# Kernel optimization log

Measured on AMD Instinct MI355X. Metric: run time of the kernel, lower is better.

Reference implementation:

```python
import jax, jax.numpy as jnp
import numpy as np

B = 16384
LATENT = 16
HID = 512
STYLE = 64
D = 10  # num_domains


def setup_inputs() -> dict:
    key = jax.random.key(0)
    ks = jax.random.split(key, 20)
    s = 0.02
    inp = {
        "z": jax.random.normal(ks[0], (B, LATENT), jnp.float32),
        "y": jax.random.randint(ks[1], (B,), 0, D, jnp.int32),
        "W0": jax.random.normal(ks[2], (LATENT, HID), jnp.float32) * s,
        "b0": jnp.zeros((HID,), jnp.float32),
        "W1": jax.random.normal(ks[3], (HID, HID), jnp.float32) * s,
        "b1": jnp.zeros((HID,), jnp.float32),
        "W2": jax.random.normal(ks[4], (HID, HID), jnp.float32) * s,
        "b2": jnp.zeros((HID,), jnp.float32),
        "W3": jax.random.normal(ks[5], (HID, HID), jnp.float32) * s,
        "b3": jnp.zeros((HID,), jnp.float32),
        "Wu1": jax.random.normal(ks[6], (D, HID, HID), jnp.float32) * s,
        "bu1": jnp.zeros((D, HID), jnp.float32),
        "Wu2": jax.random.normal(ks[7], (D, HID, HID), jnp.float32) * s,
        "bu2": jnp.zeros((D, HID), jnp.float32),
        "Wu3": jax.random.normal(ks[8], (D, HID, HID), jnp.float32) * s,
        "bu3": jnp.zeros((D, HID), jnp.float32),
        "Wo": jax.random.normal(ks[9], (D, HID, STYLE), jnp.float32) * s,
        "bo": jnp.zeros((D, STYLE), jnp.float32),
    }
    return inp


def reference(z, y, W0, b0, W1, b1, W2, b2, W3, b3,
              Wu1, bu1, Wu2, bu2, Wu3, bu3, Wo, bo):
    # shared trunk
    h = jax.nn.relu(z @ W0 + b0)
    h = jax.nn.relu(h @ W1 + b1)
    h = jax.nn.relu(h @ W2 + b2)
    h = jax.nn.relu(h @ W3 + b3)            # [B, HID]
    # all unshared heads computed densely (as in the original torch.stack)
    t = jax.nn.relu(jnp.einsum('bh,dhk->bdk', h, Wu1) + bu1)   # [B, D, HID]
    t = jax.nn.relu(jnp.einsum('bdh,dhk->bdk', t, Wu2) + bu2)
    t = jax.nn.relu(jnp.einsum('bdh,dhk->bdk', t, Wu3) + bu3)
    out = jnp.einsum('bdh,dhk->bdk', t, Wo) + bo               # [B, D, STYLE]
    # gather the branch indexed by y for each sample
    s = out[jnp.arange(z.shape[0]), y]                          # [B, STYLE]
    return s
```

## Files before the change

kernel.cpp:

```cpp
#include <hip/hip_runtime.h>

#define NB 16384
#define NDOM 10
#define HIDN 512
#define STYLE 64
#define NWIN 256

typedef short bf16x8 __attribute__((ext_vector_type(8)));
typedef float f32x16 __attribute__((ext_vector_type(16)));

#define MFMA __builtin_amdgcn_mfma_f32_32x32x16_bf16


__device__ __forceinline__ unsigned bfr_hi(float x) {
    unsigned u = __float_as_uint(x);
    return (u + 0x7fffu + ((u >> 16) & 1u)) & 0xffff0000u;
}

__device__ __forceinline__ unsigned cvtpk(float a, float b) {
    unsigned r;
    asm("v_cvt_pk_bf16_f32 %0, %1, %2" : "=v"(r) : "v"(a), "v"(b));
    return r;
}

__device__ __forceinline__ void cvhalf2(const float4& x, const float4& y, uint4& h, uint4& l) {
    float xs[8] = {x.x, x.y, x.z, x.w, y.x, y.y, y.z, y.w};
    unsigned hh[8], ll[8];
#pragma unroll
    for (int i = 0; i < 8; ++i) {
        unsigned hb = bfr_hi(xs[i]);
        hh[i] = hb;
        ll[i] = bfr_hi(xs[i] - __uint_as_float(hb));
    }
    h = make_uint4((hh[0] >> 16) | (hh[1] & 0xffff0000u), (hh[2] >> 16) | (hh[3] & 0xffff0000u),
                   (hh[4] >> 16) | (hh[5] & 0xffff0000u), (hh[6] >> 16) | (hh[7] & 0xffff0000u));
    l = make_uint4((ll[0] >> 16) | (ll[1] & 0xffff0000u), (ll[2] >> 16) | (ll[3] & 0xffff0000u),
                   (ll[4] >> 16) | (ll[5] & 0xffff0000u), (ll[6] >> 16) | (ll[7] & 0xffff0000u));
}


__global__ void k_scatter(const int* __restrict__ y, const int* __restrict__ counts,
                          int* __restrict__ cursors, int* __restrict__ rowidx) {
    __shared__ int soff[NDOM];
    if (threadIdx.x == 0) {
        int s = 0;
        for (int dd = 0; dd < NDOM; ++dd) { soff[dd] = s; s += counts[dd]; }
    }
    __syncthreads();
    int b = blockIdx.x * 256 + threadIdx.x;
    int d = y[b];
    int lane = threadIdx.x & 63;
#pragma unroll
    for (int dd = 0; dd < NDOM; ++dd) {
        unsigned long long bal = __ballot(d == dd);
        if (bal == 0ULL) continue;
        int leader = __builtin_ctzll(bal);
        int base = 0;
        if (d == dd && lane == leader)
            base = atomicAdd(&cursors[dd], (int)__popcll(bal));
        base = __shfl(base, leader);
        if (d == dd) {
            int rank = (int)__popcll(bal & ((1ULL << lane) - 1ULL));
            rowidx[soff[dd] + base + rank] = b;
        }
    }
}


__global__ void k_prep(const float* __restrict__ W1, const float* __restrict__ W2,
                       const float* __restrict__ W3, const float* __restrict__ Wu1,
                       const float* __restrict__ Wu2, const float* __restrict__ Wu3,
                       const float* __restrict__ W0, const float* __restrict__ Wo,
                       const int* __restrict__ y,
                       short* __restrict__ Wp, short* __restrict__ W0p,
                       short* __restrict__ WoP, int* __restrict__ counts)
{
    const int b = blockIdx.x;
    const int t = threadIdx.x;
    if (b < 2112) {
        __shared__ float Ld[64][68];
        const int mat = b >> 6, wq = (b >> 3) & 7, s = b & 7;
        const float* src;
        if (mat < 3) src = (mat == 0 ? W1 : (mat == 1 ? W2 : W3));
        else {
            int g = (mat - 3) / 10, d = (mat - 3) % 10;
            src = (g == 0 ? Wu1 : (g == 1 ? Wu2 : Wu3)) + (size_t)d * HIDN * HIDN;
        }
        short* dst = Wp + (size_t)mat * 262144 + wq * 32768;
#pragma unroll
        for (int i = 0; i < 4; ++i) {
            int idx = i * 256 + t;
            int row = idx >> 4, c4 = idx & 15;
            *(float4*)&Ld[row][c4 * 4] =
                *(const float4*)(src + (size_t)(s * 64 + row) * HIDN + wq * 64 + c4 * 4);
        }
        __syncthreads();
#pragma unroll
        for (int i = 0; i < 2; ++i) {
            int g = i * 256 + t;
            int ksl = g >> 7, of = (g >> 6) & 1, k8 = (g >> 5) & 1, c5 = g & 31;
            int kk = ksl * 16 + k8 * 8;
            unsigned pk[4];
#pragma unroll
            for (int j2 = 0; j2 < 4; ++j2) {
                unsigned h0 = bfr_hi(Ld[kk + 2 * j2][of * 32 + c5]);
                unsigned h1 = bfr_hi(Ld[kk + 2 * j2 + 1][of * 32 + c5]);
                pk[j2] = (h0 >> 16) | (h1 & 0xffff0000u);
            }
            int ksg = s * 4 + ksl;
            *(uint4*)(dst + ksg * 1024 + of * 512 + k8 * 256 + c5 * 8) =
                make_uint4(pk[0], pk[1], pk[2], pk[3]);
        }
    } else if (b == 2112) {
#pragma unroll
        for (int i = 0; i < 4; ++i) {
            int g = i * 256 + t;
            int wq = g >> 7, of = (g >> 6) & 1, k8 = (g >> 5) & 1, c5 = g & 31;
            int col = wq * 64 + of * 32 + c5;
            unsigned pk[4];
#pragma unroll
            for (int j2 = 0; j2 < 4; ++j2) {
                unsigned h0 = bfr_hi(W0[(size_t)(k8 * 8 + 2 * j2) * HIDN + col]);
                unsigned h1 = bfr_hi(W0[(size_t)(k8 * 8 + 2 * j2 + 1) * HIDN + col]);
                pk[j2] = (h0 >> 16) | (h1 & 0xffff0000u);
            }
            *(uint4*)(W0p + g * 8) = make_uint4(pk[0], pk[1], pk[2], pk[3]);
        }
    } else if (b < 2123) {
        const int dom = b - 2113;
        const float* src = Wo + (size_t)dom * HIDN * STYLE;
        short* dst = WoP + (size_t)dom * 32768;
#pragma unroll
        for (int i = 0; i < 16; ++i) {
            int g = i * 256 + t;
            int w1 = g >> 11, ks = (g >> 6) & 31, k8 = (g >> 5) & 1, c5 = g & 31;
            int col = w1 * 32 + c5;
            int k0 = ks * 16 + k8 * 8;
            unsigned pk[4];
#pragma unroll
            for (int j2 = 0; j2 < 4; ++j2) {
                unsigned h0 = bfr_hi(src[(size_t)(k0 + 2 * j2) * STYLE + col]);
                unsigned h1 = bfr_hi(src[(size_t)(k0 + 2 * j2 + 1) * STYLE + col]);
                pk[j2] = (h0 >> 16) | (h1 & 0xffff0000u);
            }
            *(uint4*)(dst + g * 8) = make_uint4(pk[0], pk[1], pk[2], pk[3]);
        }
    } else {
        int idx = (b - 2123) * 256 + t;
        int d = y[idx];
        int lane = t & 63;
#pragma unroll
        for (int dd = 0; dd < NDOM; ++dd) {
            unsigned long long bal = __ballot(d == dd);
            if (bal != 0ULL && d == dd && lane == __builtin_ctzll(bal))
                atomicAdd(&counts[dd], (int)__popcll(bal));
        }
    }
}


template<int NFM>
__device__ __forceinline__ void pass512(const short* __restrict__ sH,
                                        const short* __restrict__ pW,
                                        int w, int lane, f32x16 acc[2])
{
#pragma unroll
    for (int nf = 0; nf < 2; ++nf)
        if (NFM & (1 << nf))
#pragma unroll
            for (int e = 0; e < 16; ++e) acc[nf][e] = 0.f;
    const int rb = (lane & 31) * 8;
    const int lh = lane >> 5;
    const short* p = pW + (w >> 1) * 32768 + (w & 1) * 512 + lane * 8;
    bf16x8 wv[4];
#pragma unroll
    for (int d = 0; d < 4; ++d) wv[d] = *(const bf16x8*)(p + d * 1024);
    bf16x8 hb[2][2];
    const int base0 = lh * 512 + rb;
#pragma unroll
    for (int nf = 0; nf < 2; ++nf)
        if (NFM & (1 << nf)) hb[0][nf] = *(const bf16x8*)(sH + base0 + nf * 256);
#pragma unroll
    for (int ks = 0; ks < 32; ++ks) {
        const int pc = ks & 1, pn = pc ^ 1;
        bf16x8 wk = wv[ks & 3];
        if (ks < 28) wv[ks & 3] = *(const bf16x8*)(p + (ks + 4) * 1024);
        if (ks < 31) {
            const int basen = (2 * (ks + 1) + lh) * 512 + rb;
#pragma unroll
            for (int nf = 0; nf < 2; ++nf)
                if (NFM & (1 << nf)) hb[pn][nf] = *(const bf16x8*)(sH + basen + nf * 256);
        }
#pragma unroll
        for (int nf = 0; nf < 2; ++nf)
            if (NFM & (1 << nf)) acc[nf] = MFMA(wk, hb[pc][nf], acc[nf], 0, 0, 0);
    }
}

template<int NFM, bool RELU>
__device__ __forceinline__ void epi512(short* __restrict__ sH, f32x16 acc[2],
                                       const float* __restrict__ bias,
                                       int w, int lane, int rlo, int rhi)
{
    const int lh = lane >> 5;
#pragma unroll
    for (int nf = 0; nf < 2; ++nf) {
        if (!(NFM & (1 << nf))) continue;
        const int row = nf * 32 + (lane & 31);
        const bool pred = (row >= rlo && row < rhi);
        unsigned mh[4][2];
#pragma unroll
        for (int q = 0; q < 4; ++q) {
            const float4 bv = *(const float4*)&bias[w * 32 + q * 8 + lh * 4];
            float v[4];
#pragma unroll
            for (int j = 0; j < 4; ++j) {
                float x = acc[nf][q * 4 + j] + (&bv.x)[j];
                if (RELU) x = fmaxf(x, 0.f);
                v[j] = x;
            }
            mh[q][0] = cvtpk(v[0], v[1]);
            mh[q][1] = cvtpk(v[2], v[3]);
        }
#pragma unroll
        for (int t = 0; t < 2; ++t) {
            const int q = 2 * t + lh;
            const int qs = 2 * t + (lh ^ 1);
            unsigned r0 = (unsigned)__shfl_xor((int)mh[qs][0], 32);
            unsigned r1 = (unsigned)__shfl_xor((int)mh[qs][1], 32);
            uint4 line = lh == 0 ? make_uint4(mh[q][0], mh[q][1], r0, r1)
                                 : make_uint4(r0, r1, mh[q][0], mh[q][1]);
            if (pred) *(uint4*)(sH + (w * 4 + q) * 512 + row * 8) = line;
        }
    }
}

__global__ __launch_bounds__(1024, 4)
void k_fused(const float* __restrict__ z, const int* __restrict__ rowidx,
             const int* __restrict__ counts,
             const short* __restrict__ Wp, const short* __restrict__ W0p,
             const short* __restrict__ WoP,
             const float* __restrict__ b0, const float* __restrict__ b1,
             const float* __restrict__ b2, const float* __restrict__ b3,
             const float* __restrict__ bu1, const float* __restrict__ bu2,
             const float* __restrict__ bu3, const float* __restrict__ bo,
             float* __restrict__ out)
{
    __shared__ short sH[32768];
    __shared__ int soff[NDOM + 1];

    const int win = (blockIdx.x & 7) * 32 + (blockIdx.x >> 3);
    const int row0 = win * 64;
    const int tid = threadIdx.x;
    const int lane = tid & 63;
    const int w = tid >> 6;
    const int lh = lane >> 5;

    if (tid == 0) {
        int s = 0;
#pragma unroll
        for (int dd = 0; dd < NDOM; ++dd) { soff[dd] = s; s += counts[dd]; }
        soff[NDOM] = s;
    }

    f32x16 acc[2];

    {
        bf16x8 w0v = *(const bf16x8*)(W0p + (w >> 1) * 1024 + (w & 1) * 512 + lane * 8);
#pragma unroll
        for (int nf = 0; nf < 2; ++nf) {
#pragma unroll
            for (int e = 0; e < 16; ++e) acc[nf][e] = 0.f;
            const int r = nf * 32 + (lane & 31);
            const int src = rowidx[row0 + r];
            const float* zp = z + (size_t)src * 16 + lh * 8;
            float4 f0 = *(const float4*)zp;
            float4 f1 = *(const float4*)(zp + 4);
            uint4 h, l;
            cvhalf2(f0, f1, h, l);
            bf16x8 zh = *(bf16x8*)&h;
            bf16x8 zl = *(bf16x8*)&l;
            acc[nf] = MFMA(w0v, zh, acc[nf], 0, 0, 0);
            acc[nf] = MFMA(w0v, zl, acc[nf], 0, 0, 0);
        }
        epi512<3, true>(sH, acc, b0, w, lane, 0, 64);
        __syncthreads();
    }

#pragma unroll 1
    for (int m = 0; m < 3; ++m) {
        const float* bp = (m == 0) ? b1 : (m == 1) ? b2 : b3;
        pass512<3>(sH, Wp + (size_t)m * 262144, w, lane, acc);
        __syncthreads();
        epi512<3, true>(sH, acc, bp, w, lane, 0, 64);
        __syncthreads();
    }

#pragma unroll 1
    for (int L = 0; L < 3; ++L) {
        const short* WL_ = Wp + (size_t)(3 + L * 10) * 262144;
        const float* bL = (L == 0) ? bu1 : (L == 1) ? bu2 : bu3;
#pragma unroll 1
        for (int d = 0; d < NDOM; ++d) {
            int rlo = soff[d] - row0, rhi = soff[d + 1] - row0;
            rlo = rlo < 0 ? 0 : rlo;
            rhi = rhi > 64 ? 64 : rhi;
            if (rhi <= rlo) continue;
            const int nfm = (rlo < 32 ? 1 : 0) | (rhi > 32 ? 2 : 0);
            const short* pw = WL_ + (size_t)d * 262144;
            if (nfm == 3)      pass512<3>(sH, pw, w, lane, acc);
            else if (nfm == 1) pass512<1>(sH, pw, w, lane, acc);
            else               pass512<2>(sH, pw, w, lane, acc);
            __syncthreads();
            if (nfm == 3)      epi512<3, true>(sH, acc, bL + d * HIDN, w, lane, rlo, rhi);
            else if (nfm == 1) epi512<1, true>(sH, acc, bL + d * HIDN, w, lane, rlo, rhi);
            else               epi512<2, true>(sH, acc, bL + d * HIDN, w, lane, rlo, rhi);
            __syncthreads();
        }
    }

    if (w < 4) {
        const int rh = w >> 1, ch = w & 1;
        const int r = rh * 32 + (lane & 31);
#pragma unroll 1
        for (int d = 0; d < NDOM; ++d) {
            int rlo = soff[d] - row0, rhi = soff[d + 1] - row0;
            rlo = rlo < 0 ? 0 : rlo;
            rhi = rhi > 64 ? 64 : rhi;
            if (rhi <= rlo) continue;
            if (rhi <= rh * 32 || rlo >= rh * 32 + 32) continue;
            f32x16 fa;
#pragma unroll
            for (int e = 0; e < 16; ++e) fa[e] = 0.f;
            const short* pw = WoP + (size_t)d * 32768 + ch * 16384 + lane * 8;
            bf16x8 wb[4];
#pragma unroll
            for (int dd = 0; dd < 4; ++dd) wb[dd] = *(const bf16x8*)(pw + dd * 512);
            const int hbase = (rh * 32 + (lane & 31)) * 8;
#pragma unroll
            for (int ks = 0; ks < 32; ++ks) {
                bf16x8 wk = wb[ks & 3];
                if (ks < 28) wb[ks & 3] = *(const bf16x8*)(pw + (ks + 4) * 512);
                bf16x8 bhv = *(const bf16x8*)(sH + (2 * ks + lh) * 512 + hbase);
                fa = MFMA(wk, bhv, fa, 0, 0, 0);
            }
            if (r >= rlo && r < rhi) {
                const int orow = rowidx[row0 + r];
                float* op = out + (size_t)orow * STYLE + ch * 32 + lh * 4;
                const float* bop = bo + d * STYLE + ch * 32 + lh * 4;
#pragma unroll
                for (int q = 0; q < 4; ++q) {
                    float4 v;
                    v.x = fa[q * 4 + 0] + bop[q * 8 + 0];
                    v.y = fa[q * 4 + 1] + bop[q * 8 + 1];
                    v.z = fa[q * 4 + 2] + bop[q * 8 + 2];
                    v.w = fa[q * 4 + 3] + bop[q * 8 + 3];
                    *(float4*)(op + q * 8) = v;
                }
            }
        }
    }
}


extern "C" void kernel_launch(void* const* d_in, const int* in_sizes, int n_in,
                              void* d_out, int out_size, void* d_ws, size_t ws_size,
                              hipStream_t stream) {
    const float* z   = (const float*)d_in[0];
    const int*   y   = (const int*)d_in[1];
    const float* W0  = (const float*)d_in[2];
    const float* b0  = (const float*)d_in[3];
    const float* W1  = (const float*)d_in[4];
    const float* b1  = (const float*)d_in[5];
    const float* W2  = (const float*)d_in[6];
    const float* b2  = (const float*)d_in[7];
    const float* W3  = (const float*)d_in[8];
    const float* b3  = (const float*)d_in[9];
    const float* Wu1 = (const float*)d_in[10];
    const float* bu1 = (const float*)d_in[11];
    const float* Wu2 = (const float*)d_in[12];
    const float* bu2 = (const float*)d_in[13];
    const float* Wu3 = (const float*)d_in[14];
    const float* bu3 = (const float*)d_in[15];
    const float* Wo  = (const float*)d_in[16];
    const float* bo  = (const float*)d_in[17];
    float* out = (float*)d_out;

    short* Wp   = (short*)d_ws;
    short* W0p  = Wp + (size_t)33 * 262144;
    short* WoP  = W0p + 8192;
    int* rowidx  = (int*)(WoP + (size_t)10 * 32768);
    int* counts  = rowidx + NB;
    int* cursors = counts + NDOM;

    hipMemsetAsync(counts, 0, sizeof(int) * 2 * NDOM, stream);
    k_prep<<<2187, 256, 0, stream>>>(W1, W2, W3, Wu1, Wu2, Wu3, W0, Wo, y,
                                     Wp, W0p, WoP, counts);
    k_scatter<<<NB / 256, 256, 0, stream>>>(y, counts, cursors, rowidx);
    k_fused<<<NWIN, 1024, 0, stream>>>(z, rowidx, counts, Wp, W0p, WoP,
                                       b0, b1, b2, b3, bu1, bu2, bu3, bo, out);
}
```

Baseline: 162.7 us.

## Merge prep, scatter and fused MLP into one cooperative kernel with grid syncs

Replaces the memset plus three launches (weight packing, domain scatter, fused MLP) with a single cooperative kernel of 256 blocks. Weight packing and per-chunk domain counting run as a task loop, followed by a grid sync, a deterministic prefix-sum scatter done by 16 blocks, another grid sync, and then the existing fused compute. The scatter no longer uses atomics. This removes launch gaps and the memset, but packing now runs on only 256 blocks with per-slab syncs instead of 2187 small blocks, which may lengthen the prep phase, and the two grid-wide barriers add their own cost.

```diff
diff --git a/kernel.cpp b/kernel.cpp
--- a/kernel.cpp
+++ b/kernel.cpp
@@ -1,10 +1,12 @@
 #include <hip/hip_runtime.h>
+#include <hip/hip_cooperative_groups.h>
+
+namespace cg = cooperative_groups;
 
 #define NB 16384
 #define NDOM 10
 #define HIDN 512
 #define STYLE 64
-#define NWIN 256
 
 typedef short bf16x8 __attribute__((ext_vector_type(8)));
 typedef float f32x16 __attribute__((ext_vector_type(16)));
@@ -38,125 +40,16 @@
                    (ll[4] >> 16) | (ll[5] & 0xffff0000u), (ll[6] >> 16) | (ll[7] & 0xffff0000u));
 }
 
-
-__global__ void k_scatter(const int* __restrict__ y, const int* __restrict__ counts,
-                          int* __restrict__ cursors, int* __restrict__ rowidx) {
-    __shared__ int soff[NDOM];
-    if (threadIdx.x == 0) {
-        int s = 0;
-        for (int dd = 0; dd < NDOM; ++dd) { soff[dd] = s; s += counts[dd]; }
-    }
-    __syncthreads();
-    int b = blockIdx.x * 256 + threadIdx.x;
-    int d = y[b];
-    int lane = threadIdx.x & 63;
-#pragma unroll
-    for (int dd = 0; dd < NDOM; ++dd) {
-        unsigned long long bal = __ballot(d == dd);
-        if (bal == 0ULL) continue;
-        int leader = __builtin_ctzll(bal);
-        int base = 0;
-        if (d == dd && lane == leader)
-            base = atomicAdd(&cursors[dd], (int)__popcll(bal));
-        base = __shfl(base, leader);
-        if (d == dd) {
-            int rank = (int)__popcll(bal & ((1ULL << lane) - 1ULL));
-            rowidx[soff[dd] + base + rank] = b;
-        }
-    }
-}
-
-
-__global__ void k_prep(const float* __restrict__ W1, const float* __restrict__ W2,
-                       const float* __restrict__ W3, const float* __restrict__ Wu1,
-                       const float* __restrict__ Wu2, const float* __restrict__ Wu3,
-                       const float* __restrict__ W0, const float* __restrict__ Wo,
-                       const int* __restrict__ y,
-                       short* __restrict__ Wp, short* __restrict__ W0p,
-                       short* __restrict__ WoP, int* __restrict__ counts)
-{
-    const int b = blockIdx.x;
-    const int t = threadIdx.x;
-    if (b < 2112) {
-        __shared__ float Ld[64][68];
-        const int mat = b >> 6, wq = (b >> 3) & 7, s = b & 7;
-        const float* src;
-        if (mat < 3) src = (mat == 0 ? W1 : (mat == 1 ? W2 : W3));
-        else {
-            int g = (mat - 3) / 10, d = (mat - 3) % 10;
-            src = (g == 0 ? Wu1 : (g == 1 ? Wu2 : Wu3)) + (size_t)d * HIDN * HIDN;
-        }
-        short* dst = Wp + (size_t)mat * 262144 + wq * 32768;
-#pragma unroll
-        for (int i = 0; i < 4; ++i) {
-            int idx = i * 256 + t;
-            int row = idx >> 4, c4 = idx & 15;
-            *(float4*)&Ld[row][c4 * 4] =
-                *(const float4*)(src + (size_t)(s * 64 + row) * HIDN + wq * 64 + c4 * 4);
-        }
-        __syncthreads();
-#pragma unroll
-        for (int i = 0; i < 2; ++i) {
-            int g = i * 256 + t;
-            int ksl = g >> 7, of = (g >> 6) & 1, k8 = (g >> 5) & 1, c5 = g & 31;
-            int kk = ksl * 16 + k8 * 8;
-            unsigned pk[4];
-#pragma unroll
-            for (int j2 = 0; j2 < 4; ++j2) {
-                unsigned h0 = bfr_hi(Ld[kk + 2 * j2][of * 32 + c5]);
-                unsigned h1 = bfr_hi(Ld[kk + 2 * j2 + 1][of * 32 + c5]);
-                pk[j2] = (h0 >> 16) | (h1 & 0xffff0000u);
-            }
-            int ksg = s * 4 + ksl;
-            *(uint4*)(dst + ksg * 1024 + of * 512 + k8 * 256 + c5 * 8) =
-                make_uint4(pk[0], pk[1], pk[2], pk[3]);
-        }
-    } else if (b == 2112) {
-#pragma unroll
-        for (int i = 0; i < 4; ++i) {
-            int g = i * 256 + t;
-            int wq = g >> 7, of = (g >> 6) & 1, k8 = (g >> 5) & 1, c5 = g & 31;
-            int col = wq * 64 + of * 32 + c5;
-            unsigned pk[4];
-#pragma unroll
-            for (int j2 = 0; j2 < 4; ++j2) {
-                unsigned h0 = bfr_hi(W0[(size_t)(k8 * 8 + 2 * j2) * HIDN + col]);
-                unsigned h1 = bfr_hi(W0[(size_t)(k8 * 8 + 2 * j2 + 1) * HIDN + col]);
-                pk[j2] = (h0 >> 16) | (h1 & 0xffff0000u);
-            }
-            *(uint4*)(W0p + g * 8) = make_uint4(pk[0], pk[1], pk[2], pk[3]);
-        }
-    } else if (b < 2123) {
-        const int dom = b - 2113;
-        const float* src = Wo + (size_t)dom * HIDN * STYLE;
-        short* dst = WoP + (size_t)dom * 32768;
-#pragma unroll
-        for (int i = 0; i < 16; ++i) {
-            int g = i * 256 + t;
-            int w1 = g >> 11, ks = (g >> 6) & 31, k8 = (g >> 5) & 1, c5 = g & 31;
-            int col = w1 * 32 + c5;
-            int k0 = ks * 16 + k8 * 8;
-            unsigned pk[4];
-#pragma unroll
-            for (int j2 = 0; j2 < 4; ++j2) {
-                unsigned h0 = bfr_hi(src[(size_t)(k0 + 2 * j2) * STYLE + col]);
-                unsigned h1 = bfr_hi(src[(size_t)(k0 + 2 * j2 + 1) * STYLE + col]);
-                pk[j2] = (h0 >> 16) | (h1 & 0xffff0000u);
-            }
-            *(uint4*)(dst + g * 8) = make_uint4(pk[0], pk[1], pk[2], pk[3]);
-        }
-    } else {
-        int idx = (b - 2123) * 256 + t;
-        int d = y[idx];
-        int lane = t & 63;
-#pragma unroll
-        for (int dd = 0; dd < NDOM; ++dd) {
-            unsigned long long bal = __ballot(d == dd);
-            if (bal != 0ULL && d == dd && lane == __builtin_ctzll(bal))
-                atomicAdd(&counts[dd], (int)__popcll(bal));
-        }
-    }
-}
+struct KParams {
+    const float* z; const int* y;
+    const float* W0; const float* b0; const float* W1; const float* b1;
+    const float* W2; const float* b2; const float* W3; const float* b3;
+    const float* Wu1; const float* bu1; const float* Wu2; const float* bu2;
+    const float* Wu3; const float* bu3; const float* Wo; const float* bo;
+    short* Wp; short* W0p; short* WoP;
+    int* rowidx; int* partial;
+    float* out;
+};
 
 
 template<int NFM>
@@ -235,45 +128,173 @@
     }
 }
 
+
 __global__ __launch_bounds__(1024, 4)
-void k_fused(const float* __restrict__ z, const int* __restrict__ rowidx,
-             const int* __restrict__ counts,
-             const short* __restrict__ Wp, const short* __restrict__ W0p,
-             const short* __restrict__ WoP,
-             const float* __restrict__ b0, const float* __restrict__ b1,
-             const float* __restrict__ b2, const float* __restrict__ b3,
-             const float* __restrict__ bu1, const float* __restrict__ bu2,
-             const float* __restrict__ bu3, const float* __restrict__ bo,
-             float* __restrict__ out)
+void k_all(KParams P)
 {
-    __shared__ short sH[32768];
+    __shared__ __align__(16) short sH[32768];
+    __shared__ int scnt[16][NDOM];
+    __shared__ int sbase[16][NDOM];
+    __shared__ int sAux[NDOM + 1];
+    __shared__ int sPfx[NDOM];
     __shared__ int soff[NDOM + 1];
 
-    const int win = (blockIdx.x & 7) * 32 + (blockIdx.x >> 3);
-    const int row0 = win * 64;
     const int tid = threadIdx.x;
     const int lane = tid & 63;
     const int w = tid >> 6;
     const int lh = lane >> 5;
-
+    const int bid = blockIdx.x;
+
+    float* Ld = (float*)sH;
+    for (int task = bid; task < 291; task += 256) {
+        __syncthreads();
+        if (task < 264) {
+            const int mat = task >> 3, wq = task & 7;
+            const float* src;
+            if (mat < 3) src = (mat == 0 ? P.W1 : (mat == 1 ? P.W2 : P.W3));
+            else {
+                int g = (mat - 3) / 10, d = (mat - 3) % 10;
+                src = (g == 0 ? P.Wu1 : (g == 1 ? P.Wu2 : P.Wu3)) + (size_t)d * HIDN * HIDN;
+            }
+            short* dst = P.Wp + (size_t)mat * 262144 + wq * 32768;
+            for (int s = 0; s < 8; ++s) {
+                {
+                    int row = tid >> 4, c4 = tid & 15;
+                    *(float4*)&Ld[row * 68 + c4 * 4] =
+                        *(const float4*)(src + (size_t)(s * 64 + row) * HIDN + wq * 64 + c4 * 4);
+                }
+                __syncthreads();
+                if (tid < 512) {
+                    int g = tid;
+                    int ksl = g >> 7, of = (g >> 6) & 1, k8 = (g >> 5) & 1, c5 = g & 31;
+                    int kk = ksl * 16 + k8 * 8;
+                    unsigned pk[4];
+#pragma unroll
+                    for (int j2 = 0; j2 < 4; ++j2) {
+                        unsigned h0 = bfr_hi(Ld[(kk + 2 * j2) * 68 + of * 32 + c5]);
+                        unsigned h1 = bfr_hi(Ld[(kk + 2 * j2 + 1) * 68 + of * 32 + c5]);
+                        pk[j2] = (h0 >> 16) | (h1 & 0xffff0000u);
+                    }
+                    *(uint4*)(dst + (s * 4 + ksl) * 1024 + of * 512 + k8 * 256 + c5 * 8) =
+                        make_uint4(pk[0], pk[1], pk[2], pk[3]);
+                }
+                __syncthreads();
+            }
+        } else if (task == 264) {
+            int g = tid;
+            int wq = g >> 7, of = (g >> 6) & 1, k8 = (g >> 5) & 1, c5 = g & 31;
+            int col = wq * 64 + of * 32 + c5;
+            unsigned pk[4];
+#pragma unroll
+            for (int j2 = 0; j2 < 4; ++j2) {
+                unsigned h0 = bfr_hi(P.W0[(size_t)(k8 * 8 + 2 * j2) * HIDN + col]);
+                unsigned h1 = bfr_hi(P.W0[(size_t)(k8 * 8 + 2 * j2 + 1) * HIDN + col]);
+                pk[j2] = (h0 >> 16) | (h1 & 0xffff0000u);
+            }
+            *(uint4*)(P.W0p + g * 8) = make_uint4(pk[0], pk[1], pk[2], pk[3]);
+        } else if (task < 275) {
+            const int dom = task - 265;
+            const float* src = P.Wo + (size_t)dom * HIDN * STYLE;
+            short* dst = P.WoP + (size_t)dom * 32768;
+#pragma unroll
+            for (int i = 0; i < 4; ++i) {
+                int g = i * 1024 + tid;
+                int w1 = g >> 11, ks = (g >> 6) & 31, k8 = (g >> 5) & 1, c5 = g & 31;
+                int col = w1 * 32 + c5;
+                int k0 = ks * 16 + k8 * 8;
+                unsigned pk[4];
+#pragma unroll
+                for (int j2 = 0; j2 < 4; ++j2) {
+                    unsigned h0 = bfr_hi(src[(size_t)(k0 + 2 * j2) * STYLE + col]);
+                    unsigned h1 = bfr_hi(src[(size_t)(k0 + 2 * j2 + 1) * STYLE + col]);
+                    pk[j2] = (h0 >> 16) | (h1 & 0xffff0000u);
+                }
+                *(uint4*)(dst + g * 8) = make_uint4(pk[0], pk[1], pk[2], pk[3]);
+            }
+        } else {
+            const int chunk = task - 275;
+            const int d = P.y[chunk * 1024 + tid];
+#pragma unroll
+            for (int dd = 0; dd < NDOM; ++dd) {
+                unsigned long long bal = __ballot(d == dd);
+                if (lane == 0) scnt[w][dd] = (int)__popcll(bal);
+            }
+            __syncthreads();
+            if (tid < NDOM) {
+                int tot = 0;
+#pragma unroll
+                for (int c = 0; c < 16; ++c) tot += scnt[c][tid];
+                P.partial[chunk * NDOM + tid] = tot;
+            }
+        }
+    }
+
+    cg::this_grid().sync();
+
+    if (bid < 16) {
+        const int chunk = bid;
+        if (tid < NDOM) {
+            int tot = 0, pfx = 0;
+            for (int c = 0; c < 16; ++c) {
+                int v = P.partial[c * NDOM + tid];
+                if (c < chunk) pfx += v;
+                tot += v;
+            }
+            sAux[tid] = tot; sPfx[tid] = pfx;
+        }
+        __syncthreads();
+        const int i = chunk * 1024 + tid;
+        const int d = P.y[i];
+        const unsigned long long below = (1ULL << lane) - 1ULL;
+        int rnk = 0;
+#pragma unroll
+        for (int dd = 0; dd < NDOM; ++dd) {
+            unsigned long long bal = __ballot(d == dd);
+            if (d == dd) rnk = (int)__popcll(bal & below);
+            if (lane == 0) scnt[w][dd] = (int)__popcll(bal);
+        }
+        if (tid == 0) {
+            int s = 0;
+            for (int dd = 0; dd < NDOM; ++dd) { int t2 = sAux[dd]; sAux[dd] = s; s += t2; }
+        }
+        __syncthreads();
+        if (tid < NDOM) {
+            int s = 0;
+            for (int c = 0; c < 16; ++c) { sbase[c][tid] = s; s += scnt[c][tid]; }
+        }
+        __syncthreads();
+        P.rowidx[sAux[d] + sPfx[d] + sbase[w][d] + rnk] = i;
+    }
+
+    cg::this_grid().sync();
+
+    const int win = (bid & 7) * 32 + (bid >> 3);
+    const int row0 = win * 64;
+
+    if (tid < NDOM) {
+        int tot = 0;
+        for (int c = 0; c < 16; ++c) tot += P.partial[c * NDOM + tid];
+        sAux[tid] = tot;
+    }
+    __syncthreads();
     if (tid == 0) {
         int s = 0;
 #pragma unroll
-        for (int dd = 0; dd < NDOM; ++dd) { soff[dd] = s; s += counts[dd]; }
+        for (int dd = 0; dd < NDOM; ++dd) { soff[dd] = s; s += sAux[dd]; }
         soff[NDOM] = s;
     }
 
     f32x16 acc[2];
 
     {
-        bf16x8 w0v = *(const bf16x8*)(W0p + (w >> 1) * 1024 + (w & 1) * 512 + lane * 8);
+        bf16x8 w0v = *(const bf16x8*)(P.W0p + (w >> 1) * 1024 + (w & 1) * 512 + lane * 8);
 #pragma unroll
         for (int nf = 0; nf < 2; ++nf) {
 #pragma unroll
             for (int e = 0; e < 16; ++e) acc[nf][e] = 0.f;
             const int r = nf * 32 + (lane & 31);
-            const int src = rowidx[row0 + r];
-            const float* zp = z + (size_t)src * 16 + lh * 8;
+            const int src = P.rowidx[row0 + r];
+            const float* zp = P.z + (size_t)src * 16 + lh * 8;
             float4 f0 = *(const float4*)zp;
             float4 f1 = *(const float4*)(zp + 4);
             uint4 h, l;
@@ -283,14 +304,14 @@
             acc[nf] = MFMA(w0v, zh, acc[nf], 0, 0, 0);
             acc[nf] = MFMA(w0v, zl, acc[nf], 0, 0, 0);
         }
-        epi512<3, true>(sH, acc, b0, w, lane, 0, 64);
+        epi512<3, true>(sH, acc, P.b0, w, lane, 0, 64);
         __syncthreads();
     }
 
 #pragma unroll 1
     for (int m = 0; m < 3; ++m) {
-        const float* bp = (m == 0) ? b1 : (m == 1) ? b2 : b3;
-        pass512<3>(sH, Wp + (size_t)m * 262144, w, lane, acc);
+        const float* bp = (m == 0) ? P.b1 : (m == 1) ? P.b2 : P.b3;
+        pass512<3>(sH, P.Wp + (size_t)m * 262144, w, lane, acc);
         __syncthreads();
         epi512<3, true>(sH, acc, bp, w, lane, 0, 64);
         __syncthreads();
@@ -298,8 +319,8 @@
 
 #pragma unroll 1
     for (int L = 0; L < 3; ++L) {
-        const short* WL_ = Wp + (size_t)(3 + L * 10) * 262144;
-        const float* bL = (L == 0) ? bu1 : (L == 1) ? bu2 : bu3;
+        const short* WL_ = P.Wp + (size_t)(3 + L * 10) * 262144;
+        const float* bL = (L == 0) ? P.bu1 : (L == 1) ? P.bu2 : P.bu3;
 #pragma unroll 1
         for (int d = 0; d < NDOM; ++d) {
             int rlo = soff[d] - row0, rhi = soff[d + 1] - row0;
@@ -332,7 +353,7 @@
             f32x16 fa;
 #pragma unroll
             for (int e = 0; e < 16; ++e) fa[e] = 0.f;
-            const short* pw = WoP + (size_t)d * 32768 + ch * 16384 + lane * 8;
+            const short* pw = P.WoP + (size_t)d * 32768 + ch * 16384 + lane * 8;
             bf16x8 wb[4];
 #pragma unroll
             for (int dd = 0; dd < 4; ++dd) wb[dd] = *(const bf16x8*)(pw + dd * 512);
@@ -345,9 +366,9 @@
                 fa = MFMA(wk, bhv, fa, 0, 0, 0);
             }
             if (r >= rlo && r < rhi) {
-                const int orow = rowidx[row0 + r];
-                float* op = out + (size_t)orow * STYLE + ch * 32 + lh * 4;
-                const float* bop = bo + d * STYLE + ch * 32 + lh * 4;
+                const int orow = P.rowidx[row0 + r];
+                float* op = P.out + (size_t)orow * STYLE + ch * 32 + lh * 4;
+                const float* bop = P.bo + d * STYLE + ch * 32 + lh * 4;
 #pragma unroll
                 for (int q = 0; q < 4; ++q) {
                     float4 v;
@@ -366,37 +387,35 @@
 extern "C" void kernel_launch(void* const* d_in, const int* in_sizes, int n_in,
                               void* d_out, int out_size, void* d_ws, size_t ws_size,
                               hipStream_t stream) {
-    const float* z   = (const float*)d_in[0];
-    const int*   y   = (const int*)d_in[1];
-    const float* W0  = (const float*)d_in[2];
-    const float* b0  = (const float*)d_in[3];
-    const float* W1  = (const float*)d_in[4];
-    const float* b1  = (const float*)d_in[5];
-    const float* W2  = (const float*)d_in[6];
-    const float* b2  = (const float*)d_in[7];
-    const float* W3  = (const float*)d_in[8];
-    const float* b3  = (const float*)d_in[9];
-    const float* Wu1 = (const float*)d_in[10];
-    const float* bu1 = (const float*)d_in[11];
-    const float* Wu2 = (const float*)d_in[12];
-    const float* bu2 = (const float*)d_in[13];
-    const float* Wu3 = (const float*)d_in[14];
-    const float* bu3 = (const float*)d_in[15];
-    const float* Wo  = (const float*)d_in[16];
-    const float* bo  = (const float*)d_in[17];
-    float* out = (float*)d_out;
+    KParams prm;
+    prm.z   = (const float*)d_in[0];
+    prm.y   = (const int*)d_in[1];
+    prm.W0  = (const float*)d_in[2];
+    prm.b0  = (const float*)d_in[3];
+    prm.W1  = (const float*)d_in[4];
+    prm.b1  = (const float*)d_in[5];
+    prm.W2  = (const float*)d_in[6];
+    prm.b2  = (const float*)d_in[7];
+    prm.W3  = (const float*)d_in[8];
+    prm.b3  = (const float*)d_in[9];
+    prm.Wu1 = (const float*)d_in[10];
+    prm.bu1 = (const float*)d_in[11];
+    prm.Wu2 = (const float*)d_in[12];
+    prm.bu2 = (const float*)d_in[13];
+    prm.Wu3 = (const float*)d_in[14];
+    prm.bu3 = (const float*)d_in[15];
+    prm.Wo  = (const float*)d_in[16];
+    prm.bo  = (const float*)d_in[17];
+    prm.out = (float*)d_out;
 
     short* Wp   = (short*)d_ws;
     short* W0p  = Wp + (size_t)33 * 262144;
     short* WoP  = W0p + 8192;
     int* rowidx  = (int*)(WoP + (size_t)10 * 32768);
-    int* counts  = rowidx + NB;
-    int* cursors = counts + NDOM;
-
-    hipMemsetAsync(counts, 0, sizeof(int) * 2 * NDOM, stream);
-    k_prep<<<2187, 256, 0, stream>>>(W1, W2, W3, Wu1, Wu2, Wu3, W0, Wo, y,
-                                     Wp, W0p, WoP, counts);
-    k_scatter<<<NB / 256, 256, 0, stream>>>(y, counts, cursors, rowidx);
-    k_fused<<<NWIN, 1024, 0, stream>>>(z, rowidx, counts, Wp, W0p, WoP,
-                                       b0, b1, b2, b3, bu1, bu2, bu3, bo, out);
-}
+    int* partial = rowidx + NB;
+    prm.Wp = Wp; prm.W0p = W0p; prm.WoP = WoP;
+    prm.rowidx = rowidx; prm.partial = partial;
+
+    void* args[] = { &prm };
+    hipLaunchCooperativeKernel((void*)k_all, dim3(256), dim3(1024), args, 0, stream);
+}
```

Measured after the change: 176.3 us. 8.4% more time.
